# Kernel tuning notes

Measured on AMD Instinct MI355X. Metric: run time of the kernel, lower is better.

The kernel has to match this reference:

```python
import jax, jax.numpy as jnp
import numpy as np

EPS = 1e-15


def setup_inputs() -> dict:
    key = jax.random.key(0)
    k1, k2 = jax.random.split(key)
    B, N, M, D = 32, 512, 64, 128  # D=128 hard-coded in original (np.zeros(128))
    videos_repr = jax.random.normal(k1, (B, N, D), dtype=jnp.float32)
    sentences_repr = jax.random.normal(k2, (B, M, D), dtype=jnp.float32)
    return {"videos_repr": videos_repr, "sentences_repr": sentences_repr}


def reference(videos_repr, sentences_repr):
    """Vectorized all-pairs (training=True) path of MomentVideo.call.

    videos_repr: [B, N, D], sentences_repr: [B, M, D].
    Returns (sum_scores_videos [B,B], sum_scores_sentences [B,B]).
    """
    V, S = videos_repr, sentences_repr
    nv = jnp.linalg.norm(V, axis=-1)  # [B, N]
    ns = jnp.linalg.norm(S, axis=-1)  # [B, M]

    # Co-attention cosine-similarity matrix for every (video i, sentence j) pair.
    # C[i,j,n,m] = <V[i,n], S[j,m]> / (||V[i,n]|| * ||S[j,m]|| + eps)
    C = jnp.einsum('ind,jmd->ijnm', V, S) / (
        nv[:, None, :, None] * ns[None, :, None, :] + EPS)

    Ps = jax.nn.softmax(C, axis=3)  # softmax over sentence words (axis=1 in per-pair matrix)
    Pv = jax.nn.softmax(C, axis=2)  # softmax over video segments (axis=0 in per-pair matrix)

    # sentence_attention[i,j,n] = sum_m Ps[i,j,n,m] * S[j,m]
    A = jnp.einsum('ijnm,jmd->ijnd', Ps, S)   # [B, B, N, D]
    # video_attention[i,j,m] = sum_n Pv[i,j,n,m] * V[i,n]
    Bt = jnp.einsum('ijnm,ind->ijmd', Pv, V)  # [B, B, M, D]

    na = jnp.linalg.norm(A, axis=-1)   # [B, B, N]
    nb = jnp.linalg.norm(Bt, axis=-1)  # [B, B, M]

    # cosine(V[i,n], A[i,j,n]) and cosine(S[j,m], Bt[i,j,m])
    sv = jnp.einsum('ind,ijnd->ijn', V, A) / (nv[:, None, :] * na + EPS)
    ss = jnp.einsum('jmd,ijmd->ijm', S, Bt) / (ns[None, :, :] * nb + EPS)

    sum_scores_videos = sv.mean(axis=-1)          # [B, B], [i, j]
    sum_scores_sentences = ss.mean(axis=-1).T     # transposed as in original
    return sum_scores_videos, sum_scores_sentences
```

## Files before the change

### kernel.cpp

```cpp
#include <hip/hip_runtime.h>
#include <hip/hip_bf16.h>
#include <math.h>

#define BB 32
#define NN 512
#define MM 64
#define DD 128
#define TILE 64
#define NTILES 8

typedef __attribute__((ext_vector_type(8))) short s8v;
typedef __attribute__((ext_vector_type(4))) float f4v;
typedef __attribute__((ext_vector_type(4))) unsigned short u4v;
typedef __attribute__((ext_vector_type(8))) unsigned short u8v;

#define MFMA(a, b, c) __builtin_amdgcn_mfma_f32_16x16x32_bf16((a), (b), (c), 0, 0, 0)

__device__ inline unsigned short f2b(float f) {
  union { __hip_bfloat16 b; unsigned short u; } cv;
  cv.b = __float2bfloat16(f);
  return cv.u;
}

__device__ inline int idxV(int r, int k)  { return r * 128 + (k ^ ((r & 7) << 3)); }
__device__ inline int idx64(int r, int k) { return r * 64  + (k ^ ((r & 7) << 3)); }

struct __align__(16) SMem {
  unsigned short VA[64 * 128];
  union { unsigned short Sb[64 * 128]; unsigned short VT[128 * 64]; };
  union { unsigned short Gb[64 * 64];  unsigned short Eb[64 * 64]; };
  unsigned short ET[64 * 64];
  float red_sv[2][16][16][4];
  float red_qp[2][16][16][4];
  float red_s[8][64];
  float nv_l[2][64];
  float rnv_l[64];
  float ns_l[64], rns_l[64];
  float ssnum[64];
};

extern "C" __global__ void __launch_bounds__(512, 2)
mv_mfma3(const float* __restrict__ Vg, const float* __restrict__ Sg,
         float* __restrict__ out)
{
  extern __shared__ char smraw[];
  SMem& sm = *reinterpret_cast<SMem*>(smraw);

  const int t    = threadIdx.x;
  const int lane = t & 63;
  const int w    = t >> 6;
  const int l15  = lane & 15;
  const int g    = lane >> 4;
  const int bi   = blockIdx.x >> 5;
  const int bj   = blockIdx.x & 31;

  const float* Vi = Vg + (size_t)bi * NN * DD;
  const float* Sj = Sg + (size_t)bj * MM * DD;

  const int nb  = w >> 1;
  const int hf  = w & 1;
  const int cB0 = hf * 32 + l15;
  const int cB1 = cB0 + 16;

  const int r = t >> 3;
  const int c = t & 7;

  {
    const float* Sp = Sj + r * DD + c * 16;
    float4 f0 = reinterpret_cast<const float4*>(Sp)[0];
    float4 f1 = reinterpret_cast<const float4*>(Sp)[1];
    float4 f2 = reinterpret_cast<const float4*>(Sp)[2];
    float4 f3 = reinterpret_cast<const float4*>(Sp)[3];
    u8v lo = { f2b(f0.x), f2b(f0.y), f2b(f0.z), f2b(f0.w),
               f2b(f1.x), f2b(f1.y), f2b(f1.z), f2b(f1.w) };
    u8v hi = { f2b(f2.x), f2b(f2.y), f2b(f2.z), f2b(f2.w),
               f2b(f3.x), f2b(f3.y), f2b(f3.z), f2b(f3.w) };
    *reinterpret_cast<u8v*>(&sm.Sb[idxV(r, c * 16)])     = lo;
    *reinterpret_cast<u8v*>(&sm.Sb[idxV(r, c * 16 + 8)]) = hi;
    float s = f0.x*f0.x + f0.y*f0.y + f0.z*f0.z + f0.w*f0.w
            + f1.x*f1.x + f1.y*f1.y + f1.z*f1.z + f1.w*f1.w
            + f2.x*f2.x + f2.y*f2.y + f2.z*f2.z + f2.w*f2.w
            + f3.x*f3.x + f3.y*f3.y + f3.z*f3.z + f3.w*f3.w;
    s += __shfl_xor(s, 1, 64);
    s += __shfl_xor(s, 2, 64);
    s += __shfl_xor(s, 4, 64);
    if (c == 0) {
      const float rs = rsqrtf(s);
      sm.ns_l[r] = s * rs;
      sm.rns_l[r] = rs;
    }
  }
  if (t < 64) sm.ssnum[t] = 0.f;
  __syncthreads();

  {
    f4v g0 = {0.f,0.f,0.f,0.f}, g1 = {0.f,0.f,0.f,0.f};
    #pragma unroll
    for (int ks = 0; ks < 4; ++ks) {
      s8v a  = *reinterpret_cast<const s8v*>(&sm.Sb[idxV(nb * 16 + l15, ks * 32 + g * 8)]);
      s8v b0 = *reinterpret_cast<const s8v*>(&sm.Sb[idxV(cB0,          ks * 32 + g * 8)]);
      s8v b1 = *reinterpret_cast<const s8v*>(&sm.Sb[idxV(cB1,          ks * 32 + g * 8)]);
      g0 = MFMA(a, b0, g0);
      g1 = MFMA(a, b1, g1);
    }
    #pragma unroll
    for (int q = 0; q < 4; ++q) {
      const int row = nb * 16 + g * 4 + q;
      sm.Gb[idx64(row, cB0)] = f2b(g0[q]);
      sm.Gb[idx64(row, cB1)] = f2b(g1[q]);
    }
  }
  __syncthreads();

  s8v sfr0[4], sfr1[4], gfr0[2], gfr1[2];
  #pragma unroll
  for (int ks = 0; ks < 4; ++ks) {
    sfr0[ks] = *reinterpret_cast<const s8v*>(&sm.Sb[idxV(cB0, ks * 32 + g * 8)]);
    sfr1[ks] = *reinterpret_cast<const s8v*>(&sm.Sb[idxV(cB1, ks * 32 + g * 8)]);
  }
  #pragma unroll
  for (int ks = 0; ks < 2; ++ks) {
    gfr0[ks] = *reinterpret_cast<const s8v*>(&sm.Gb[idx64(cB0, ks * 32 + g * 8)]);
    gfr1[ks] = *reinterpret_cast<const s8v*>(&sm.Gb[idx64(cB1, ks * 32 + g * 8)]);
  }
  const float rns0r = sm.rns_l[cB0];
  const float rns1r = sm.rns_l[cB1];

  f4v bt4[4] = {{0.f,0.f,0.f,0.f},{0.f,0.f,0.f,0.f},{0.f,0.f,0.f,0.f},{0.f,0.f,0.f,0.f}};
  float svacc = 0.f;

  for (int tt = 0; tt < NTILES; ++tt) {
    __syncthreads();

    {
      const float* Vr = Vi + (size_t)tt * TILE * DD + r * DD + c * 16;
      float4 f0 = reinterpret_cast<const float4*>(Vr)[0];
      float4 f1 = reinterpret_cast<const float4*>(Vr)[1];
      float4 f2 = reinterpret_cast<const float4*>(Vr)[2];
      float4 f3 = reinterpret_cast<const float4*>(Vr)[3];
      unsigned short vb16[16] = {
        f2b(f0.x), f2b(f0.y), f2b(f0.z), f2b(f0.w),
        f2b(f1.x), f2b(f1.y), f2b(f1.z), f2b(f1.w),
        f2b(f2.x), f2b(f2.y), f2b(f2.z), f2b(f2.w),
        f2b(f3.x), f2b(f3.y), f2b(f3.z), f2b(f3.w) };
      u8v lo = { vb16[0], vb16[1], vb16[2], vb16[3], vb16[4], vb16[5], vb16[6], vb16[7] };
      u8v hi = { vb16[8], vb16[9], vb16[10], vb16[11], vb16[12], vb16[13], vb16[14], vb16[15] };
      *reinterpret_cast<u8v*>(&sm.VA[idxV(r, c * 16)])     = lo;
      *reinterpret_cast<u8v*>(&sm.VA[idxV(r, c * 16 + 8)]) = hi;
      #pragma unroll
      for (int q = 0; q < 8; ++q) {
        const int adr = ((c * 16 + q) << 6) + (r ^ (((q ^ c) & 7) << 3));
        sm.VT[adr]       = vb16[q];
        sm.VT[adr + 512] = vb16[q + 8];
      }
      float s = f0.x*f0.x + f0.y*f0.y + f0.z*f0.z + f0.w*f0.w
              + f1.x*f1.x + f1.y*f1.y + f1.z*f1.z + f1.w*f1.w
              + f2.x*f2.x + f2.y*f2.y + f2.z*f2.z + f2.w*f2.w
              + f3.x*f3.x + f3.y*f3.y + f3.z*f3.z + f3.w*f3.w;
      s += __shfl_xor(s, 1, 64);
      s += __shfl_xor(s, 2, 64);
      s += __shfl_xor(s, 4, 64);
      if (c == 0) {
        const float rs = rsqrtf(s);
        sm.nv_l[tt & 1][r] = s * rs;
        sm.rnv_l[r] = rs;
      }
    }
    if (tt > 0 && t < 64) {
      const int rg = t >> 2, qq = t & 3;
      float sv_n = 0.f, qf = 0.f;
      #pragma unroll
      for (int l = 0; l < 16; ++l) {
        sv_n += sm.red_sv[0][rg][l][qq] + sm.red_sv[1][rg][l][qq];
        qf   += sm.red_qp[0][rg][l][qq] + sm.red_qp[1][rg][l][qq];
      }
      svacc += sv_n / (sm.nv_l[(tt & 1) ^ 1][t] * sqrtf(qf));
      const int hh = t >> 5;
      float ssn = 0.f;
      #pragma unroll
      for (int n2 = 0; n2 < 4; ++n2) ssn += sm.red_s[n2 * 2 + hh][t];
      sm.ssnum[t] += ssn;
    }
    __syncthreads();

    f4v a0 = {0.f,0.f,0.f,0.f}, a1 = {0.f,0.f,0.f,0.f};
    {
      const int ar = nb * 16 + l15;
      #pragma unroll
      for (int ks = 0; ks < 4; ++ks) {
        s8v av = *reinterpret_cast<const s8v*>(&sm.VA[idxV(ar, ks * 32 + g * 8)]);
        a0 = MFMA(av, sfr0[ks], a0);
        a1 = MFMA(av, sfr1[ks], a1);
      }
    }
    float e0[4], e1[4];
    {
      const float4 rv = *reinterpret_cast<const float4*>(&sm.rnv_l[nb * 16 + g * 4]);
      float sv4[4];
      float ss0 = 0.f, ss1 = 0.f;
      unsigned short eb0[4], eb1[4];
      #pragma unroll
      for (int q = 0; q < 4; ++q) {
        const float rvq = (q == 0) ? rv.x : (q == 1) ? rv.y : (q == 2) ? rv.z : rv.w;
        const float c0 = a0[q] * (rvq * rns0r);
        const float c1 = a1[q] * (rvq * rns1r);
        const float e0q = __expf(c0);
        const float e1q = __expf(c1);
        const float w0 = e0q * a0[q], w1 = e1q * a1[q];
        sv4[q] = w0 + w1;
        ss0 += w0; ss1 += w1;
        eb0[q] = f2b(e0q); eb1[q] = f2b(e1q);
        const int row = nb * 16 + g * 4 + q;
        sm.Eb[idx64(row, cB0)] = eb0[q];
        sm.Eb[idx64(row, cB1)] = eb1[q];
        e0[q] = e0q; e1[q] = e1q;
      }
      u4v et0 = { eb0[0], eb0[1], eb0[2], eb0[3] };
      u4v et1 = { eb1[0], eb1[1], eb1[2], eb1[3] };
      *reinterpret_cast<u4v*>(&sm.ET[idx64(cB0, nb * 16 + g * 4)]) = et0;
      *reinterpret_cast<u4v*>(&sm.ET[idx64(cB1, nb * 16 + g * 4)]) = et1;
      *reinterpret_cast<float4*>(&sm.red_sv[hf][nb * 4 + g][l15][0]) =
          make_float4(sv4[0], sv4[1], sv4[2], sv4[3]);
      ss0 += __shfl_xor(ss0, 16, 64);  ss0 += __shfl_xor(ss0, 32, 64);
      ss1 += __shfl_xor(ss1, 16, 64);  ss1 += __shfl_xor(ss1, 32, 64);
      if (g == 0) { sm.red_s[w][cB0] = ss0; sm.red_s[w][cB1] = ss1; }
    }
    __syncthreads();

    {
      f4v fa0 = {0.f,0.f,0.f,0.f}, fa1 = {0.f,0.f,0.f,0.f};
      #pragma unroll
      for (int ks = 0; ks < 2; ++ks) {
        s8v ea = *reinterpret_cast<const s8v*>(&sm.Eb[idx64(nb * 16 + l15, ks * 32 + g * 8)]);
        fa0 = MFMA(ea, gfr0[ks], fa0);
        fa1 = MFMA(ea, gfr1[ks], fa1);
      }
      *reinterpret_cast<float4*>(&sm.red_qp[hf][nb * 4 + g][l15][0]) =
          make_float4(e0[0]*fa0[0] + e1[0]*fa1[0], e0[1]*fa0[1] + e1[1]*fa1[1],
                      e0[2]*fa0[2] + e1[2]*fa1[2], e0[3]*fa0[3] + e1[3]*fa1[3]);
    }
    {
      const int xr = l15 & 7;
      #pragma unroll
      for (int ks = 0; ks < 2; ++ks) {
        s8v pa = *reinterpret_cast<const s8v*>(&sm.ET[idx64(nb * 16 + l15, ks * 32 + g * 8)]);
        const int k0 = ks * 32 + g * 8;
        #pragma unroll
        for (int dt = 0; dt < 4; ++dt) {
          const int rowv = (hf * 4 + dt) * 16 + l15;
          const int elem = (rowv << 6) + (k0 ^ (((xr ^ (hf * 4 + dt)) & 7) << 3));
          s8v vb = *reinterpret_cast<const s8v*>(&sm.VT[elem]);
          bt4[dt] = MFMA(pa, vb, bt4[dt]);
        }
      }
    }
  }

  __syncthreads();
  if (t < 64) {
    const int rg = t >> 2, qq = t & 3;
    float sv_n = 0.f, qf = 0.f;
    #pragma unroll
    for (int l = 0; l < 16; ++l) {
      sv_n += sm.red_sv[0][rg][l][qq] + sm.red_sv[1][rg][l][qq];
      qf   += sm.red_qp[0][rg][l][qq] + sm.red_qp[1][rg][l][qq];
    }
    svacc += sv_n / (sm.nv_l[1][t] * sqrtf(qf));
    const int hh = t >> 5;
    float ssn = 0.f;
    #pragma unroll
    for (int n2 = 0; n2 < 4; ++n2) ssn += sm.red_s[n2 * 2 + hh][t];
    sm.ssnum[t] += ssn;
  }
  __syncthreads();
  {
    float bq[4];
    #pragma unroll
    for (int q = 0; q < 4; ++q)
      bq[q] = bt4[0][q]*bt4[0][q] + bt4[1][q]*bt4[1][q]
            + bt4[2][q]*bt4[2][q] + bt4[3][q]*bt4[3][q];
    *reinterpret_cast<float4*>(&sm.red_qp[hf][nb * 4 + g][l15][0]) =
        make_float4(bq[0], bq[1], bq[2], bq[3]);
  }
  __syncthreads();
  if (t < 64) {
    const int rg = t >> 2, qq = t & 3;
    float btq = 0.f;
    #pragma unroll
    for (int l = 0; l < 16; ++l)
      btq += sm.red_qp[0][rg][l][qq] + sm.red_qp[1][rg][l][qq];
    float ssv = sm.ssnum[t] / (sm.ns_l[t] * sqrtf(btq));
    float svv = svacc;
    #pragma unroll
    for (int msk = 32; msk >= 1; msk >>= 1) {
      ssv += __shfl_xor(ssv, msk, 64);
      svv += __shfl_xor(svv, msk, 64);
    }
    if (t == 0) {
      out[bi * BB + bj]           = svv * (1.0f / NN);
      out[BB * BB + bj * BB + bi] = ssv * (1.0f / MM);
    }
  }
}

extern "C" void kernel_launch(void* const* d_in, const int* in_sizes, int n_in,
                              void* d_out, int out_size, void* d_ws, size_t ws_size,
                              hipStream_t stream) {
  const float* V = (const float*)d_in[0];
  const float* S = (const float*)d_in[1];
  float* out = (float*)d_out;

  static_assert(sizeof(SMem) <= 80 * 1024, "need 2 blocks/CU");
  hipFuncSetAttribute(reinterpret_cast<const void*>(mv_mfma3),
                      hipFuncAttributeMaxDynamicSharedMemorySize,
                      (int)sizeof(SMem));
  mv_mfma3<<<dim3(BB * BB), dim3(512), sizeof(SMem), stream>>>(V, S, out);
}
```

Baseline: 145.9 us.

## Split bf16 conversion into a prep kernel and prefetch pre-swizzled tiles

Adds a prep kernel that converts V and S to bf16 once, builds the swizzled row-major and transposed tile images, precomputes the norms and the S Gram matrix, and writes them all to workspace. Before this, each of the 1024 pair blocks redid that conversion and transpose for its V tiles. The main kernel now copies the preformatted tiles straight into LDS, register-prefetches the next tile while the current one computes, and pads the reduction buffers. The cost is a second launch and extra global traffic for the intermediates.

Result: faster. 132.4 us (-9.2%).

```diff
diff --git a/kernel.cpp b/kernel.cpp
--- a/kernel.cpp
+++ b/kernel.cpp
@@ -25,58 +25,46 @@
 __device__ inline int idxV(int r, int k)  { return r * 128 + (k ^ ((r & 7) << 3)); }
 __device__ inline int idx64(int r, int k) { return r * 64  + (k ^ ((r & 7) << 3)); }
 
-struct __align__(16) SMem {
-  unsigned short VA[64 * 128];
-  union { unsigned short Sb[64 * 128]; unsigned short VT[128 * 64]; };
-  union { unsigned short Gb[64 * 64];  unsigned short Eb[64 * 64]; };
-  unsigned short ET[64 * 64];
-  float red_sv[2][16][16][4];
-  float red_qp[2][16][16][4];
-  float red_s[8][64];
-  float nv_l[2][64];
-  float rnv_l[64];
-  float ns_l[64], rns_l[64];
-  float ssnum[64];
+struct __align__(16) PSM {
+  unsigned short A[64 * 128];
+  unsigned short B[128 * 64];
 };
 
 extern "C" __global__ void __launch_bounds__(512, 2)
-mv_mfma3(const float* __restrict__ Vg, const float* __restrict__ Sg,
-         float* __restrict__ out)
+mv_prep(const float* __restrict__ Vg, const float* __restrict__ Sg,
+        unsigned short* __restrict__ VAg, unsigned short* __restrict__ VTg,
+        unsigned short* __restrict__ Sbg, unsigned short* __restrict__ Gbg,
+        float* __restrict__ nvg, float* __restrict__ rnvg,
+        float* __restrict__ nsg, float* __restrict__ rnsg)
 {
   extern __shared__ char smraw[];
-  SMem& sm = *reinterpret_cast<SMem*>(smraw);
-
-  const int t    = threadIdx.x;
-  const int lane = t & 63;
-  const int w    = t >> 6;
-  const int l15  = lane & 15;
-  const int g    = lane >> 4;
-  const int bi   = blockIdx.x >> 5;
-  const int bj   = blockIdx.x & 31;
-
-  const float* Vi = Vg + (size_t)bi * NN * DD;
-  const float* Sj = Sg + (size_t)bj * MM * DD;
-
-  const int nb  = w >> 1;
-  const int hf  = w & 1;
-  const int cB0 = hf * 32 + l15;
-  const int cB1 = cB0 + 16;
-
-  const int r = t >> 3;
-  const int c = t & 7;
-
-  {
-    const float* Sp = Sj + r * DD + c * 16;
-    float4 f0 = reinterpret_cast<const float4*>(Sp)[0];
-    float4 f1 = reinterpret_cast<const float4*>(Sp)[1];
-    float4 f2 = reinterpret_cast<const float4*>(Sp)[2];
-    float4 f3 = reinterpret_cast<const float4*>(Sp)[3];
-    u8v lo = { f2b(f0.x), f2b(f0.y), f2b(f0.z), f2b(f0.w),
-               f2b(f1.x), f2b(f1.y), f2b(f1.z), f2b(f1.w) };
-    u8v hi = { f2b(f2.x), f2b(f2.y), f2b(f2.z), f2b(f2.w),
-               f2b(f3.x), f2b(f3.y), f2b(f3.z), f2b(f3.w) };
-    *reinterpret_cast<u8v*>(&sm.Sb[idxV(r, c * 16)])     = lo;
-    *reinterpret_cast<u8v*>(&sm.Sb[idxV(r, c * 16 + 8)]) = hi;
+  PSM& sm = *reinterpret_cast<PSM*>(smraw);
+  const int t = threadIdx.x;
+  const int r = t >> 3, c = t & 7;
+  const int bid = blockIdx.x;
+
+  if (bid < 256) {
+    const int i = bid >> 3, tt = bid & 7;
+    const float* Vr = Vg + ((size_t)i * NN + tt * TILE + r) * DD + c * 16;
+    float4 f0 = reinterpret_cast<const float4*>(Vr)[0];
+    float4 f1 = reinterpret_cast<const float4*>(Vr)[1];
+    float4 f2 = reinterpret_cast<const float4*>(Vr)[2];
+    float4 f3 = reinterpret_cast<const float4*>(Vr)[3];
+    unsigned short vb16[16] = {
+      f2b(f0.x), f2b(f0.y), f2b(f0.z), f2b(f0.w),
+      f2b(f1.x), f2b(f1.y), f2b(f1.z), f2b(f1.w),
+      f2b(f2.x), f2b(f2.y), f2b(f2.z), f2b(f2.w),
+      f2b(f3.x), f2b(f3.y), f2b(f3.z), f2b(f3.w) };
+    u8v lo = { vb16[0], vb16[1], vb16[2], vb16[3], vb16[4], vb16[5], vb16[6], vb16[7] };
+    u8v hi = { vb16[8], vb16[9], vb16[10], vb16[11], vb16[12], vb16[13], vb16[14], vb16[15] };
+    *reinterpret_cast<u8v*>(&sm.A[idxV(r, c * 16)])     = lo;
+    *reinterpret_cast<u8v*>(&sm.A[idxV(r, c * 16 + 8)]) = hi;
+    #pragma unroll
+    for (int q = 0; q < 8; ++q) {
+      const int adr = ((c * 16 + q) << 6) + (r ^ (((q ^ c) & 7) << 3));
+      sm.B[adr]       = vb16[q];
+      sm.B[adr + 512] = vb16[q + 8];
+    }
     float s = f0.x*f0.x + f0.y*f0.y + f0.z*f0.z + f0.w*f0.w
             + f1.x*f1.x + f1.y*f1.y + f1.z*f1.z + f1.w*f1.w
             + f2.x*f2.x + f2.y*f2.y + f2.z*f2.z + f2.w*f2.w
@@ -86,100 +74,164 @@
     s += __shfl_xor(s, 4, 64);
     if (c == 0) {
       const float rs = rsqrtf(s);
-      sm.ns_l[r] = s * rs;
-      sm.rns_l[r] = rs;
-    }
-  }
-  if (t < 64) sm.ssnum[t] = 0.f;
-  __syncthreads();
-
+      nvg [i * NN + tt * TILE + r] = s * rs;
+      rnvg[i * NN + tt * TILE + r] = rs;
+    }
+    __syncthreads();
+    unsigned short* dA = VAg + (size_t)bid * 8192;
+    unsigned short* dB = VTg + (size_t)bid * 8192;
+    *reinterpret_cast<u8v*>(&dA[t * 8])        = *reinterpret_cast<u8v*>(&sm.A[t * 8]);
+    *reinterpret_cast<u8v*>(&dA[4096 + t * 8]) = *reinterpret_cast<u8v*>(&sm.A[4096 + t * 8]);
+    *reinterpret_cast<u8v*>(&dB[t * 8])        = *reinterpret_cast<u8v*>(&sm.B[t * 8]);
+    *reinterpret_cast<u8v*>(&dB[4096 + t * 8]) = *reinterpret_cast<u8v*>(&sm.B[4096 + t * 8]);
+  } else {
+    const int j = bid - 256;
+    const float* Sp = Sg + ((size_t)j * MM + r) * DD + c * 16;
+    float4 f0 = reinterpret_cast<const float4*>(Sp)[0];
+    float4 f1 = reinterpret_cast<const float4*>(Sp)[1];
+    float4 f2 = reinterpret_cast<const float4*>(Sp)[2];
+    float4 f3 = reinterpret_cast<const float4*>(Sp)[3];
+    u8v lo = { f2b(f0.x), f2b(f0.y), f2b(f0.z), f2b(f0.w),
+               f2b(f1.x), f2b(f1.y), f2b(f1.z), f2b(f1.w) };
+    u8v hi = { f2b(f2.x), f2b(f2.y), f2b(f2.z), f2b(f2.w),
+               f2b(f3.x), f2b(f3.y), f2b(f3.z), f2b(f3.w) };
+    *reinterpret_cast<u8v*>(&sm.A[idxV(r, c * 16)])     = lo;
+    *reinterpret_cast<u8v*>(&sm.A[idxV(r, c * 16 + 8)]) = hi;
+    float s = f0.x*f0.x + f0.y*f0.y + f0.z*f0.z + f0.w*f0.w
+            + f1.x*f1.x + f1.y*f1.y + f1.z*f1.z + f1.w*f1.w
+            + f2.x*f2.x + f2.y*f2.y + f2.z*f2.z + f2.w*f2.w
+            + f3.x*f3.x + f3.y*f3.y + f3.z*f3.z + f3.w*f3.w;
+    s += __shfl_xor(s, 1, 64);
+    s += __shfl_xor(s, 2, 64);
+    s += __shfl_xor(s, 4, 64);
+    if (c == 0) {
+      const float rs = rsqrtf(s);
+      nsg [j * MM + r] = s * rs;
+      rnsg[j * MM + r] = rs;
+    }
+    __syncthreads();
+    {
+      const int lane = t & 63, w = t >> 6, l15 = lane & 15, g = lane >> 4;
+      const int nb = w >> 1, hf = w & 1, cB0 = hf * 32 + l15, cB1 = cB0 + 16;
+      f4v g0 = {0.f,0.f,0.f,0.f}, g1 = {0.f,0.f,0.f,0.f};
+      #pragma unroll
+      for (int ks = 0; ks < 4; ++ks) {
+        s8v a  = *reinterpret_cast<const s8v*>(&sm.A[idxV(nb * 16 + l15, ks * 32 + g * 8)]);
+        s8v b0 = *reinterpret_cast<const s8v*>(&sm.A[idxV(cB0,          ks * 32 + g * 8)]);
+        s8v b1 = *reinterpret_cast<const s8v*>(&sm.A[idxV(cB1,          ks * 32 + g * 8)]);
+        g0 = MFMA(a, b0, g0);
+        g1 = MFMA(a, b1, g1);
+      }
+      #pragma unroll
+      for (int q = 0; q < 4; ++q) {
+        const int row = nb * 16 + g * 4 + q;
+        sm.B[idx64(row, cB0)] = f2b(g0[q]);
+        sm.B[idx64(row, cB1)] = f2b(g1[q]);
+      }
+    }
+    __syncthreads();
+    unsigned short* dS = Sbg + (size_t)j * 8192;
+    *reinterpret_cast<u8v*>(&dS[r * 128 + c * 16])     = *reinterpret_cast<u8v*>(&sm.A[idxV(r, c * 16)]);
+    *reinterpret_cast<u8v*>(&dS[r * 128 + c * 16 + 8]) = *reinterpret_cast<u8v*>(&sm.A[idxV(r, c * 16 + 8)]);
+    unsigned short* dG = Gbg + (size_t)j * 4096;
+    *reinterpret_cast<u8v*>(&dG[r * 64 + c * 8]) = *reinterpret_cast<u8v*>(&sm.B[idx64(r, c * 8)]);
+  }
+}
+
+struct __align__(16) SMem2 {
+  unsigned short VA[8192];
+  unsigned short VT[8192];
+  unsigned short Eb[4096];
+  unsigned short ET[4096];
+  float RSV[32 * 68];
+  float RQP[32 * 68];
+  float RS [8 * 68];
+  float nv_lds[512];
+  float rnv_lds[512];
+};
+
+extern "C" __global__ void __launch_bounds__(512, 2)
+mv_main(const unsigned short* __restrict__ VAg, const unsigned short* __restrict__ VTg,
+        const unsigned short* __restrict__ Sbg, const unsigned short* __restrict__ Gbg,
+        const float* __restrict__ nvg, const float* __restrict__ rnvg,
+        const float* __restrict__ nsg, const float* __restrict__ rnsg,
+        float* __restrict__ out)
+{
+  extern __shared__ char smraw[];
+  SMem2& sm = *reinterpret_cast<SMem2*>(smraw);
+
+  const int t    = threadIdx.x;
+  const int lane = t & 63;
+  const int w    = t >> 6;
+  const int l15  = lane & 15;
+  const int g    = lane >> 4;
+  const int bi   = blockIdx.x >> 5;
+  const int bj   = blockIdx.x & 31;
+
+  const int nb  = w >> 1;
+  const int hf  = w & 1;
+  const int cB0 = hf * 32 + l15;
+  const int cB1 = cB0 + 16;
+
+  sm.nv_lds[t]  = nvg [bi * NN + t];
+  sm.rnv_lds[t] = rnvg[bi * NN + t];
+
+  s8v sfr0[4], sfr1[4], gfr0[2], gfr1[2];
   {
-    f4v g0 = {0.f,0.f,0.f,0.f}, g1 = {0.f,0.f,0.f,0.f};
+    const unsigned short* Sj = Sbg + (size_t)bj * 8192;
     #pragma unroll
     for (int ks = 0; ks < 4; ++ks) {
-      s8v a  = *reinterpret_cast<const s8v*>(&sm.Sb[idxV(nb * 16 + l15, ks * 32 + g * 8)]);
-      s8v b0 = *reinterpret_cast<const s8v*>(&sm.Sb[idxV(cB0,          ks * 32 + g * 8)]);
-      s8v b1 = *reinterpret_cast<const s8v*>(&sm.Sb[idxV(cB1,          ks * 32 + g * 8)]);
-      g0 = MFMA(a, b0, g0);
-      g1 = MFMA(a, b1, g1);
-    }
-    #pragma unroll
-    for (int q = 0; q < 4; ++q) {
-      const int row = nb * 16 + g * 4 + q;
-      sm.Gb[idx64(row, cB0)] = f2b(g0[q]);
-      sm.Gb[idx64(row, cB1)] = f2b(g1[q]);
-    }
-  }
-  __syncthreads();
-
-  s8v sfr0[4], sfr1[4], gfr0[2], gfr1[2];
-  #pragma unroll
-  for (int ks = 0; ks < 4; ++ks) {
-    sfr0[ks] = *reinterpret_cast<const s8v*>(&sm.Sb[idxV(cB0, ks * 32 + g * 8)]);
-    sfr1[ks] = *reinterpret_cast<const s8v*>(&sm.Sb[idxV(cB1, ks * 32 + g * 8)]);
-  }
-  #pragma unroll
-  for (int ks = 0; ks < 2; ++ks) {
-    gfr0[ks] = *reinterpret_cast<const s8v*>(&sm.Gb[idx64(cB0, ks * 32 + g * 8)]);
-    gfr1[ks] = *reinterpret_cast<const s8v*>(&sm.Gb[idx64(cB1, ks * 32 + g * 8)]);
-  }
-  const float rns0r = sm.rns_l[cB0];
-  const float rns1r = sm.rns_l[cB1];
+      sfr0[ks] = *reinterpret_cast<const s8v*>(&Sj[cB0 * 128 + ks * 32 + g * 8]);
+      sfr1[ks] = *reinterpret_cast<const s8v*>(&Sj[cB1 * 128 + ks * 32 + g * 8]);
+    }
+    const unsigned short* Gj = Gbg + (size_t)bj * 4096;
+    #pragma unroll
+    for (int ks = 0; ks < 2; ++ks) {
+      gfr0[ks] = *reinterpret_cast<const s8v*>(&Gj[cB0 * 64 + ks * 32 + g * 8]);
+      gfr1[ks] = *reinterpret_cast<const s8v*>(&Gj[cB1 * 64 + ks * 32 + g * 8]);
+    }
+  }
+  const float rns0r = rnsg[bj * MM + cB0];
+  const float rns1r = rnsg[bj * MM + cB1];
+
+  const unsigned short* VAi = VAg + (size_t)(bi * 8) * 8192;
+  const unsigned short* VTi = VTg + (size_t)(bi * 8) * 8192;
+  u8v p0 = *reinterpret_cast<const u8v*>(&VAi[t * 8]);
+  u8v p1 = *reinterpret_cast<const u8v*>(&VAi[4096 + t * 8]);
+  u8v p2 = *reinterpret_cast<const u8v*>(&VTi[t * 8]);
+  u8v p3 = *reinterpret_cast<const u8v*>(&VTi[4096 + t * 8]);
 
   f4v bt4[4] = {{0.f,0.f,0.f,0.f},{0.f,0.f,0.f,0.f},{0.f,0.f,0.f,0.f},{0.f,0.f,0.f,0.f}};
-  float svacc = 0.f;
-
+  float svacc = 0.f, ssacc = 0.f;
+
+  #pragma unroll 1
   for (int tt = 0; tt < NTILES; ++tt) {
     __syncthreads();
-
-    {
-      const float* Vr = Vi + (size_t)tt * TILE * DD + r * DD + c * 16;
-      float4 f0 = reinterpret_cast<const float4*>(Vr)[0];
-      float4 f1 = reinterpret_cast<const float4*>(Vr)[1];
-      float4 f2 = reinterpret_cast<const float4*>(Vr)[2];
-      float4 f3 = reinterpret_cast<const float4*>(Vr)[3];
-      unsigned short vb16[16] = {
-        f2b(f0.x), f2b(f0.y), f2b(f0.z), f2b(f0.w),
-        f2b(f1.x), f2b(f1.y), f2b(f1.z), f2b(f1.w),
-        f2b(f2.x), f2b(f2.y), f2b(f2.z), f2b(f2.w),
-        f2b(f3.x), f2b(f3.y), f2b(f3.z), f2b(f3.w) };
-      u8v lo = { vb16[0], vb16[1], vb16[2], vb16[3], vb16[4], vb16[5], vb16[6], vb16[7] };
-      u8v hi = { vb16[8], vb16[9], vb16[10], vb16[11], vb16[12], vb16[13], vb16[14], vb16[15] };
-      *reinterpret_cast<u8v*>(&sm.VA[idxV(r, c * 16)])     = lo;
-      *reinterpret_cast<u8v*>(&sm.VA[idxV(r, c * 16 + 8)]) = hi;
-      #pragma unroll
-      for (int q = 0; q < 8; ++q) {
-        const int adr = ((c * 16 + q) << 6) + (r ^ (((q ^ c) & 7) << 3));
-        sm.VT[adr]       = vb16[q];
-        sm.VT[adr + 512] = vb16[q + 8];
-      }
-      float s = f0.x*f0.x + f0.y*f0.y + f0.z*f0.z + f0.w*f0.w
-              + f1.x*f1.x + f1.y*f1.y + f1.z*f1.z + f1.w*f1.w
-              + f2.x*f2.x + f2.y*f2.y + f2.z*f2.z + f2.w*f2.w
-              + f3.x*f3.x + f3.y*f3.y + f3.z*f3.z + f3.w*f3.w;
-      s += __shfl_xor(s, 1, 64);
-      s += __shfl_xor(s, 2, 64);
-      s += __shfl_xor(s, 4, 64);
-      if (c == 0) {
-        const float rs = rsqrtf(s);
-        sm.nv_l[tt & 1][r] = s * rs;
-        sm.rnv_l[r] = rs;
-      }
+    *reinterpret_cast<u8v*>(&sm.VA[t * 8])        = p0;
+    *reinterpret_cast<u8v*>(&sm.VA[4096 + t * 8]) = p1;
+    *reinterpret_cast<u8v*>(&sm.VT[t * 8])        = p2;
+    *reinterpret_cast<u8v*>(&sm.VT[4096 + t * 8]) = p3;
+    if (tt < 7) {
+      const unsigned short* a = VAi + (size_t)(tt + 1) * 8192;
+      const unsigned short* b = VTi + (size_t)(tt + 1) * 8192;
+      p0 = *reinterpret_cast<const u8v*>(&a[t * 8]);
+      p1 = *reinterpret_cast<const u8v*>(&a[4096 + t * 8]);
+      p2 = *reinterpret_cast<const u8v*>(&b[t * 8]);
+      p3 = *reinterpret_cast<const u8v*>(&b[4096 + t * 8]);
     }
     if (tt > 0 && t < 64) {
-      const int rg = t >> 2, qq = t & 3;
+      const int rg = t >> 2, qq = t & 3, hh = t >> 5;
       float sv_n = 0.f, qf = 0.f;
       #pragma unroll
       for (int l = 0; l < 16; ++l) {
-        sv_n += sm.red_sv[0][rg][l][qq] + sm.red_sv[1][rg][l][qq];
-        qf   += sm.red_qp[0][rg][l][qq] + sm.red_qp[1][rg][l][qq];
-      }
-      svacc += sv_n / (sm.nv_l[(tt & 1) ^ 1][t] * sqrtf(qf));
-      const int hh = t >> 5;
+        sv_n += sm.RSV[rg * 68 + l * 4 + qq] + sm.RSV[(16 + rg) * 68 + l * 4 + qq];
+        qf   += sm.RQP[rg * 68 + l * 4 + qq] + sm.RQP[(16 + rg) * 68 + l * 4 + qq];
+      }
+      svacc += sv_n / (sm.nv_lds[(tt - 1) * TILE + t] * sqrtf(qf));
       float ssn = 0.f;
       #pragma unroll
-      for (int n2 = 0; n2 < 4; ++n2) ssn += sm.red_s[n2 * 2 + hh][t];
-      sm.ssnum[t] += ssn;
+      for (int n2 = 0; n2 < 4; ++n2) ssn += sm.RS[(n2 * 2 + hh) * 68 + t];
+      ssacc += ssn;
     }
     __syncthreads();
 
@@ -195,7 +247,7 @@
     }
     float e0[4], e1[4];
     {
-      const float4 rv = *reinterpret_cast<const float4*>(&sm.rnv_l[nb * 16 + g * 4]);
+      const float4 rv = *reinterpret_cast<const float4*>(&sm.rnv_lds[tt * TILE + nb * 16 + g * 4]);
       float sv4[4];
       float ss0 = 0.f, ss1 = 0.f;
       unsigned short eb0[4], eb1[4];
@@ -219,11 +271,11 @@
       u4v et1 = { eb1[0], eb1[1], eb1[2], eb1[3] };
       *reinterpret_cast<u4v*>(&sm.ET[idx64(cB0, nb * 16 + g * 4)]) = et0;
       *reinterpret_cast<u4v*>(&sm.ET[idx64(cB1, nb * 16 + g * 4)]) = et1;
-      *reinterpret_cast<float4*>(&sm.red_sv[hf][nb * 4 + g][l15][0]) =
+      *reinterpret_cast<float4*>(&sm.RSV[(hf * 16 + nb * 4 + g) * 68 + l15 * 4]) =
           make_float4(sv4[0], sv4[1], sv4[2], sv4[3]);
       ss0 += __shfl_xor(ss0, 16, 64);  ss0 += __shfl_xor(ss0, 32, 64);
       ss1 += __shfl_xor(ss1, 16, 64);  ss1 += __shfl_xor(ss1, 32, 64);
-      if (g == 0) { sm.red_s[w][cB0] = ss0; sm.red_s[w][cB1] = ss1; }
+      if (g == 0) { sm.RS[w * 68 + cB0] = ss0; sm.RS[w * 68 + cB1] = ss1; }
     }
     __syncthreads();
 
@@ -235,7 +287,7 @@
         fa0 = MFMA(ea, gfr0[ks], fa0);
         fa1 = MFMA(ea, gfr1[ks], fa1);
       }
-      *reinterpret_cast<float4*>(&sm.red_qp[hf][nb * 4 + g][l15][0]) =
+      *reinterpret_cast<float4*>(&sm.RQP[(hf * 16 + nb * 4 + g) * 68 + l15 * 4]) =
           make_float4(e0[0]*fa0[0] + e1[0]*fa1[0], e0[1]*fa0[1] + e1[1]*fa1[1],
                       e0[2]*fa0[2] + e1[2]*fa1[2], e0[3]*fa0[3] + e1[3]*fa1[3]);
     }
@@ -258,19 +310,18 @@
 
   __syncthreads();
   if (t < 64) {
-    const int rg = t >> 2, qq = t & 3;
+    const int rg = t >> 2, qq = t & 3, hh = t >> 5;
     float sv_n = 0.f, qf = 0.f;
     #pragma unroll
     for (int l = 0; l < 16; ++l) {
-      sv_n += sm.red_sv[0][rg][l][qq] + sm.red_sv[1][rg][l][qq];
-      qf   += sm.red_qp[0][rg][l][qq] + sm.red_qp[1][rg][l][qq];
-    }
-    svacc += sv_n / (sm.nv_l[1][t] * sqrtf(qf));
-    const int hh = t >> 5;
+      sv_n += sm.RSV[rg * 68 + l * 4 + qq] + sm.RSV[(16 + rg) * 68 + l * 4 + qq];
+      qf   += sm.RQP[rg * 68 + l * 4 + qq] + sm.RQP[(16 + rg) * 68 + l * 4 + qq];
+    }
+    svacc += sv_n / (sm.nv_lds[7 * TILE + t] * sqrtf(qf));
     float ssn = 0.f;
     #pragma unroll
-    for (int n2 = 0; n2 < 4; ++n2) ssn += sm.red_s[n2 * 2 + hh][t];
-    sm.ssnum[t] += ssn;
+    for (int n2 = 0; n2 < 4; ++n2) ssn += sm.RS[(n2 * 2 + hh) * 68 + t];
+    ssacc += ssn;
   }
   __syncthreads();
   {
@@ -279,7 +330,7 @@
     for (int q = 0; q < 4; ++q)
       bq[q] = bt4[0][q]*bt4[0][q] + bt4[1][q]*bt4[1][q]
             + bt4[2][q]*bt4[2][q] + bt4[3][q]*bt4[3][q];
-    *reinterpret_cast<float4*>(&sm.red_qp[hf][nb * 4 + g][l15][0]) =
+    *reinterpret_cast<float4*>(&sm.RQP[(hf * 16 + nb * 4 + g) * 68 + l15 * 4]) =
         make_float4(bq[0], bq[1], bq[2], bq[3]);
   }
   __syncthreads();
@@ -288,8 +339,8 @@
     float btq = 0.f;
     #pragma unroll
     for (int l = 0; l < 16; ++l)
-      btq += sm.red_qp[0][rg][l][qq] + sm.red_qp[1][rg][l][qq];
-    float ssv = sm.ssnum[t] / (sm.ns_l[t] * sqrtf(btq));
+      btq += sm.RQP[rg * 68 + l * 4 + qq] + sm.RQP[(16 + rg) * 68 + l * 4 + qq];
+    float ssv = ssacc / (nsg[bj * MM + t] * sqrtf(btq));
     float svv = svacc;
     #pragma unroll
     for (int msk = 32; msk >= 1; msk >>= 1) {
@@ -310,9 +361,25 @@
   const float* S = (const float*)d_in[1];
   float* out = (float*)d_out;
 
-  static_assert(sizeof(SMem) <= 80 * 1024, "need 2 blocks/CU");
-  hipFuncSetAttribute(reinterpret_cast<const void*>(mv_mfma3),
-                      hipFuncAttributeMaxDynamicSharedMemorySize,
-                      (int)sizeof(SMem));
-  mv_mfma3<<<dim3(BB * BB), dim3(512), sizeof(SMem), stream>>>(V, S, out);
+  char* ws = (char*)d_ws;
+  unsigned short* VAg = (unsigned short*)(ws + 0);
+  unsigned short* VTg = (unsigned short*)(ws + 4194304);
+  unsigned short* Sbg = (unsigned short*)(ws + 8388608);
+  unsigned short* Gbg = (unsigned short*)(ws + 8912896);
+  float* nvg  = (float*)(ws + 9175040);
+  float* rnvg = (float*)(ws + 9240576);
+  float* nsg  = (float*)(ws + 9306112);
+  float* rnsg = (float*)(ws + 9314304);
+
+  static_assert(sizeof(PSM)  <= 160 * 1024, "prep LDS");
+  static_assert(sizeof(SMem2) <= 80 * 1024, "main LDS: need 2 blocks/CU");
+  hipFuncSetAttribute(reinterpret_cast<const void*>(mv_prep),
+                      hipFuncAttributeMaxDynamicSharedMemorySize, (int)sizeof(PSM));
+  hipFuncSetAttribute(reinterpret_cast<const void*>(mv_main),
+                      hipFuncAttributeMaxDynamicSharedMemorySize, (int)sizeof(SMem2));
+
+  mv_prep<<<dim3(288), dim3(512), sizeof(PSM), stream>>>(
+      V, S, VAg, VTg, Sbg, Gbg, nvg, rnvg, nsg, rnsg);
+  mv_main<<<dim3(BB * BB), dim3(512), sizeof(SMem2), stream>>>(
+      VAg, VTg, Sbg, Gbg, nvg, rnvg, nsg, rnsg, out);
 }
```
